# Optimization experiments

Hardware: AMD Instinct MI355X
Metric: run time of the kernel (lower is better)

Reference implementation:

```python
import jax, jax.numpy as jnp
import numpy as np
import math
from jax import lax

A_BICUBIC = -0.75  # PyTorch bicubic coefficient


def _bicubic_resize_matrix(out_n, in_n):
    """Dense [out_n, in_n] matrix implementing 1D bicubic resize (half-pixel,
    align_corners=False, border-replicated taps) exactly like F.interpolate."""
    a = A_BICUBIC
    src = (np.arange(out_n) + 0.5) * (in_n / out_n) - 0.5
    i0 = np.floor(src).astype(np.int64)
    t = src - i0
    M = np.zeros((out_n, in_n), dtype=np.float32)
    for k in range(-1, 3):
        idx = np.clip(i0 + k, 0, in_n - 1)
        d = np.abs(t - k)
        w = np.where(d <= 1.0, (a + 2) * d**3 - (a + 3) * d**2 + 1.0,
                     np.where(d < 2.0, a * d**3 - 5 * a * d**2 + 8 * a * d - 4 * a, 0.0))
        np.add.at(M, (np.arange(out_n), idx), w)
    return jnp.asarray(M)


def _relative_position_index(w):
    coords = np.stack(np.meshgrid(np.arange(w), np.arange(w), indexing='ij'))  # [2,w,w]
    cf = coords.reshape(2, -1)
    rel = (cf[:, :, None] - cf[:, None, :]).transpose(1, 2, 0)  # [w^2,w^2,2]
    rel[..., 0] += w - 1
    rel[..., 1] += w - 1
    rel[..., 0] *= 2 * w - 1
    return rel.sum(-1)  # [w^2, w^2]


def _grid_sample_bilinear(img, grid):
    """img: [G,d,Hi,Wi]; grid: [G,Ho,Wo,2] (x,y) in [-1,1].
    Bilinear, padding_mode='zeros', align_corners=False."""
    G, d, Hi, Wi = img.shape
    Ho, Wo = grid.shape[1:3]
    gx = (grid[..., 0] + 1.0) * (Wi * 0.5) - 0.5
    gy = (grid[..., 1] + 1.0) * (Hi * 0.5) - 0.5
    x0 = jnp.floor(gx)
    y0 = jnp.floor(gy)
    imgf = img.reshape(G, d, Hi * Wi)
    out = jnp.zeros((G, d, Ho * Wo), img.dtype)
    for dy in (0, 1):
        for dx in (0, 1):
            xi = x0 + dx
            yi = y0 + dy
            w = (1.0 - jnp.abs(gx - xi)) * (1.0 - jnp.abs(gy - yi))
            valid = (xi >= 0) & (xi < Wi) & (yi >= 0) & (yi < Hi)
            xic = jnp.clip(xi, 0, Wi - 1).astype(jnp.int32)
            yic = jnp.clip(yi, 0, Hi - 1).astype(jnp.int32)
            flat = (yic * Wi + xic).reshape(G, 1, Ho * Wo)
            v = jnp.take_along_axis(imgf, flat, axis=2)  # [G,d,HoWo]
            out = out + v * (w * valid).reshape(G, 1, Ho * Wo)
    return out.reshape(G, d, Ho, Wo)


def deformable_attention(x, q_w, q_b, k_w, k_b, v_w, v_b, o_w, o_b, dw_w, dw_b, off_w, bias_table, offset_scale=2.0):
    B, N, C = x.shape
    H = W = int(math.sqrt(N))
    heads = off_w.shape[0] // 2
    hd = C // heads
    wsz = (int(math.isqrt(bias_table.shape[0])) + 1) // 2  # (2w-1)^2 -> w

    xi = x.reshape(B, H, W, C).transpose(0, 3, 1, 2)  # [B,C,H,W]

    def conv1x1(t, w, b=None):
        y = jnp.einsum('bchw,oc->bohw', t, w)
        return y if b is None else y + b[None, :, None, None]

    Q = conv1x1(xi, q_w, q_b)
    K = conv1x1(xi, k_w, k_b)
    V = conv1x1(xi, v_w, v_b)

    # offset network: depthwise 5x5 conv -> GELU -> 1x1 -> tanh -> *scale
    h = lax.conv_general_dilated(xi, dw_w, (1, 1), 'SAME', feature_group_count=C,
                                 dimension_numbers=('NCHW', 'OIHW', 'NCHW'))
    h = jax.nn.gelu(h + dw_b[None, :, None, None], approximate=False)
    offsets = jnp.tanh(conv1x1(h, off_w)) * offset_scale  # [B,2*heads,H,W]
    offsets = offsets.reshape(B, heads, 2, H, W).transpose(0, 1, 3, 4, 2)  # [B,n,H,W,2]

    gy, gx = jnp.meshgrid(jnp.linspace(-1.0, 1.0, H), jnp.linspace(-1.0, 1.0, W), indexing='ij')
    grid = jnp.stack((gx, gy), axis=-1)  # [H,W,2]
    samp = jnp.clip(grid[None, None] + offsets, -1.0, 1.0).reshape(B * heads, H, W, 2)

    Kh = K.reshape(B * heads, hd, H, W)
    Vh = V.reshape(B * heads, hd, H, W)
    Ks = _grid_sample_bilinear(Kh, samp).reshape(B, heads, hd, N).transpose(0, 1, 3, 2)  # [B,n,N,d]
    Vs = _grid_sample_bilinear(Vh, samp).reshape(B, heads, hd, N).transpose(0, 1, 3, 2)
    Qh = Q.reshape(B, heads, hd, N).transpose(0, 1, 3, 2)  # [B,n,N,d]

    scores = jnp.einsum('bhid,bhjd->bhij', Qh, Ks) / math.sqrt(hd)

    # relative bias: table lookup on static index, bicubic upsample w^2 -> N
    rpi = _relative_position_index(wsz)  # static numpy [w^2,w^2]
    bias0 = bias_table[jnp.asarray(rpi.reshape(-1)), 0].reshape(wsz * wsz, wsz * wsz)
    M = _bicubic_resize_matrix(N, wsz * wsz)
    bias = M @ bias0 @ M.T  # [N,N]
    scores = scores + bias[None, None]

    probs = jax.nn.softmax(scores, axis=-1)
    out = jnp.einsum('bhij,bhjd->bhid', probs, Vs)  # [B,n,N,d]
    out = out.transpose(0, 1, 3, 2).reshape(B, C, H, W)  # b (h d) p q
    out = conv1x1(out, o_w, o_b)
    return out.reshape(B, C, N).transpose(0, 2, 1)  # [B,N,C]


def setup_inputs() -> dict:
    key = jax.random.key(0)
    ks = jax.random.split(key, 16)
    B, N, C = 4, 1024, 512
    heads, wsz, kk = 8, 8, 5
    s = 0.02
    return {
        'x': jax.random.normal(ks[0], (B, N, C), jnp.float32),
        'q_w': jax.random.normal(ks[1], (C, C), jnp.float32) * s,
        'q_b': jax.random.normal(ks[2], (C,), jnp.float32) * s,
        'k_w': jax.random.normal(ks[3], (C, C), jnp.float32) * s,
        'k_b': jax.random.normal(ks[4], (C,), jnp.float32) * s,
        'v_w': jax.random.normal(ks[5], (C, C), jnp.float32) * s,
        'v_b': jax.random.normal(ks[6], (C,), jnp.float32) * s,
        'o_w': jax.random.normal(ks[7], (C, C), jnp.float32) * s,
        'o_b': jax.random.normal(ks[8], (C,), jnp.float32) * s,
        'dw_w': jax.random.normal(ks[9], (C, 1, kk, kk), jnp.float32) * s,
        'dw_b': jax.random.normal(ks[10], (C,), jnp.float32) * s,
        'off_w': jax.random.normal(ks[11], (2 * heads, C), jnp.float32) * s,
        'bias_table': jax.random.normal(ks[12], ((2 * wsz - 1) ** 2, 1), jnp.float32),
    }


def reference(x, q_w, q_b, k_w, k_b, v_w, v_b, o_w, o_b, dw_w, dw_b, off_w, bias_table):
    return deformable_attention(x, q_w, q_b, k_w, k_b, v_w, v_b, o_w, o_b, dw_w, dw_b, off_w, bias_table)
```

## Files before the change

kernel.cpp:

```cpp
#include <hip/hip_runtime.h>
#include <math.h>

typedef unsigned short ushort;
typedef __attribute__((ext_vector_type(8))) short bf16x8;
typedef __attribute__((ext_vector_type(4))) float f32x4;

#define MFMA16(a, b, c) __builtin_amdgcn_mfma_f32_16x16x32_bf16(a, b, c, 0, 0, 0)
#define GLOAD16(g, l)                                                   \
  __builtin_amdgcn_global_load_lds(                                     \
      (const __attribute__((address_space(1))) unsigned int*)(g),       \
      (__attribute__((address_space(3))) unsigned int*)(l), 16, 0, 0)

__device__ __forceinline__ ushort f2bf(float f) {
  unsigned u = __float_as_uint(f);
  u += 0x7FFFu + ((u >> 16) & 1u);
  return (ushort)(u >> 16);
}
__device__ __forceinline__ float bf2f(ushort b) {
  return __uint_as_float(((unsigned)b) << 16);
}
__device__ __forceinline__ unsigned pk_bf16(float a, float b) {
  unsigned u;
  asm("v_cvt_pk_bf16_f32 %0, %1, %2" : "=v"(u) : "v"(a), "v"(b));
  return u;
}

__global__ __launch_bounds__(256) void split_hi(
    const float* __restrict__ in, ushort* __restrict__ hi, int n4) {
  int i = blockIdx.x * 256 + threadIdx.x;
  if (i >= n4) return;
  float4 v = ((const float4*)in)[i];
  ushort4 h;
  h.x = f2bf(v.x); h.y = f2bf(v.y); h.z = f2bf(v.z); h.w = f2bf(v.w);
  ((ushort4*)hi)[i] = h;
}

__global__ __launch_bounds__(256) void prep_weights(
    const float* __restrict__ q_w, const float* __restrict__ k_w,
    const float* __restrict__ v_w, const float* __restrict__ o_w,
    const float* __restrict__ dw_w, ushort* __restrict__ Wq,
    ushort* __restrict__ Wk, ushort* __restrict__ Wv,
    ushort* __restrict__ Woh, ushort* __restrict__ Wol,
    float* __restrict__ dwT) {
  int blk = blockIdx.x;
  if (blk < 1024) {
    int grp = blk >> 8;
    int i = (blk & 255) * 256 + threadIdx.x;
    if (grp < 3) {
      const float* in = grp == 0 ? q_w : grp == 1 ? k_w : v_w;
      ushort* hi = grp == 0 ? Wq : grp == 1 ? Wk : Wv;
      float4 v = ((const float4*)in)[i];
      ushort4 h;
      h.x = f2bf(v.x); h.y = f2bf(v.y); h.z = f2bf(v.z); h.w = f2bf(v.w);
      ((ushort4*)hi)[i] = h;
    } else {
      float4 v = ((const float4*)o_w)[i];
      ushort4 h, l;
      h.x = f2bf(v.x); l.x = f2bf(v.x - bf2f(h.x));
      h.y = f2bf(v.y); l.y = f2bf(v.y - bf2f(h.y));
      h.z = f2bf(v.z); l.z = f2bf(v.z - bf2f(h.z));
      h.w = f2bf(v.w); l.w = f2bf(v.w - bf2f(h.w));
      ((ushort4*)Woh)[i] = h;
      ((ushort4*)Wol)[i] = l;
    }
  } else {
    int c = (blk - 1024) * 256 + threadIdx.x;
    #pragma unroll
    for (int k = 0; k < 25; ++k) dwT[k * 512 + c] = dw_w[c * 25 + k];
  }
}

__global__ __launch_bounds__(256) void gemm_qkv(
    const ushort* __restrict__ X, const ushort* __restrict__ Wq,
    const ushort* __restrict__ Wk, const ushort* __restrict__ Wv,
    const float* __restrict__ b0, const float* __restrict__ b1,
    const float* __restrict__ b2, ushort* __restrict__ Qo,
    ushort* __restrict__ Ko, ushort* __restrict__ Vo) {
  __shared__ ushort lds[12288];
  ushort* sA = lds;
  ushort* sB = lds + 8192;
  int which = blockIdx.x >> 3;
  int n0 = (blockIdx.x & 7) * 64;
  int m0 = blockIdx.y * 128;
  const ushort* W; const float* bb; ushort* Y; float scale;
  if (which == 0)      { W = Wq; bb = b0; Y = Qo; scale = 0.125f; }
  else if (which == 1) { W = Wk; bb = b1; Y = Ko; scale = 1.0f; }
  else                 { W = Wv; bb = b2; Y = Vo; scale = 1.0f; }

  int tid = threadIdx.x;
  int lane = tid & 63;
  int w = tid >> 6;
  int wr = (w >> 1) * 64;
  int wc = (w & 1) * 32;
  int l8r = lane >> 3;
  int sll = ((lane & 7) ^ l8r) << 3;
  int l16 = lane & 15, lq = lane >> 4;

  f32x4 acc[4][2];
  f32x4 zero = {0.f, 0.f, 0.f, 0.f};
  #pragma unroll
  for (int m = 0; m < 4; ++m)
    #pragma unroll
    for (int n = 0; n < 2; ++n) acc[m][n] = zero;

  for (int kt = 0; kt < 8; ++kt) {
    int kk = kt * 64;
    __syncthreads();
    #pragma unroll
    for (int q = 0; q < 4; ++q) {
      int ci = w * 4 + q;
      GLOAD16(X + (size_t)(m0 + ci * 8 + l8r) * 512 + kk + sll, sA + ci * 512);
    }
    #pragma unroll
    for (int q = 0; q < 2; ++q) {
      int ci = w * 2 + q;
      GLOAD16(W + (size_t)(n0 + ci * 8 + l8r) * 512 + kk + sll, sB + ci * 512);
    }
    __syncthreads();
    #pragma unroll
    for (int ks = 0; ks < 2; ++ks) {
      int slot = ks * 4 + lq;
      bf16x8 a[4], bvv[2];
      #pragma unroll
      for (int m = 0; m < 4; ++m) {
        int r = wr + m * 16 + l16;
        a[m] = *(const bf16x8*)&sA[r * 64 + ((slot ^ (r & 7)) << 3)];
      }
      #pragma unroll
      for (int n = 0; n < 2; ++n) {
        int r = wc + n * 16 + l16;
        bvv[n] = *(const bf16x8*)&sB[r * 64 + ((slot ^ (r & 7)) << 3)];
      }
      #pragma unroll
      for (int m = 0; m < 4; ++m)
        #pragma unroll
        for (int n = 0; n < 2; ++n)
          acc[m][n] = MFMA16(a[m], bvv[n], acc[m][n]);
    }
  }
  #pragma unroll
  for (int n = 0; n < 2; ++n) {
    int col = n0 + wc + n * 16 + l16;
    float bv = bb[col];
    #pragma unroll
    for (int m = 0; m < 4; ++m) {
      #pragma unroll
      for (int j = 0; j < 4; ++j) {
        int row = m0 + wr + m * 16 + lq * 4 + j;
        Y[(size_t)row * 512 + col] = f2bf((acc[m][n][j] + bv) * scale);
      }
    }
  }
}

__global__ __launch_bounds__(256) void gemm_mfma(
    const ushort* __restrict__ Ahi, const ushort* __restrict__ Alo,
    const ushort* __restrict__ Bhi, const ushort* __restrict__ Blo,
    const float* __restrict__ bias, float* __restrict__ Y) {
  __shared__ ushort lds[24576];
  ushort* sAhi = lds;
  ushort* sAlo = lds + 8192;
  ushort* sBhi = lds + 16384;
  ushort* sBlo = lds + 20480;
  int m0 = blockIdx.y * 128, n0 = blockIdx.x * 64;
  int tid = threadIdx.x;
  int lane = tid & 63;
  int w = tid >> 6;
  int wr = (w >> 1) * 64;
  int wc = (w & 1) * 32;
  int l8r = lane >> 3;
  int sll = ((lane & 7) ^ l8r) << 3;
  int l16 = lane & 15, lq = lane >> 4;

  f32x4 acc[4][2];
  f32x4 zero = {0.f, 0.f, 0.f, 0.f};
  #pragma unroll
  for (int m = 0; m < 4; ++m)
    #pragma unroll
    for (int n = 0; n < 2; ++n) acc[m][n] = zero;

  for (int kt = 0; kt < 8; ++kt) {
    int kk = kt * 64;
    __syncthreads();
    #pragma unroll
    for (int q = 0; q < 4; ++q) {
      int ci = w * 4 + q;
      size_t go = (size_t)(m0 + ci * 8 + l8r) * 512 + kk + sll;
      GLOAD16(Ahi + go, sAhi + ci * 512);
      GLOAD16(Alo + go, sAlo + ci * 512);
    }
    #pragma unroll
    for (int q = 0; q < 2; ++q) {
      int ci = w * 2 + q;
      size_t go = (size_t)(n0 + ci * 8 + l8r) * 512 + kk + sll;
      GLOAD16(Bhi + go, sBhi + ci * 512);
      GLOAD16(Blo + go, sBlo + ci * 512);
    }
    __syncthreads();
    #pragma unroll
    for (int ks = 0; ks < 2; ++ks) {
      int slot = ks * 4 + lq;
      bf16x8 ah[4], al[4], bh[2], bl[2];
      #pragma unroll
      for (int m = 0; m < 4; ++m) {
        int r = wr + m * 16 + l16;
        int ph = (slot ^ (r & 7)) << 3;
        ah[m] = *(const bf16x8*)&sAhi[r * 64 + ph];
        al[m] = *(const bf16x8*)&sAlo[r * 64 + ph];
      }
      #pragma unroll
      for (int n = 0; n < 2; ++n) {
        int r = wc + n * 16 + l16;
        int ph = (slot ^ (r & 7)) << 3;
        bh[n] = *(const bf16x8*)&sBhi[r * 64 + ph];
        bl[n] = *(const bf16x8*)&sBlo[r * 64 + ph];
      }
      #pragma unroll
      for (int m = 0; m < 4; ++m)
        #pragma unroll
        for (int n = 0; n < 2; ++n) {
          acc[m][n] = MFMA16(ah[m], bh[n], acc[m][n]);
          acc[m][n] = MFMA16(ah[m], bl[n], acc[m][n]);
          acc[m][n] = MFMA16(al[m], bh[n], acc[m][n]);
        }
    }
  }
  #pragma unroll
  for (int n = 0; n < 2; ++n) {
    int col = n0 + wc + n * 16 + l16;
    float bv = bias[col];
    #pragma unroll
    for (int m = 0; m < 4; ++m) {
      #pragma unroll
      for (int j = 0; j < 4; ++j) {
        int row = m0 + wr + m * 16 + lq * 4 + j;
        Y[(size_t)row * 512 + col] = acc[m][n][j] + bv;
      }
    }
  }
}

__global__ __launch_bounds__(256) void offset_net2(
    const float* __restrict__ x, const float* __restrict__ dwT,
    const float* __restrict__ dw_b, const float* __restrict__ off_w,
    float* __restrict__ samp) {
  __shared__ float wT[16][516];
  __shared__ float hT[16][516];
  __shared__ float ofs[16][16];
  int x0 = blockIdx.x * 16;
  int y = blockIdx.y;
  int b = blockIdx.z;
  int tid = threadIdx.x;

  for (int e = tid; e < 2048; e += 256) {
    int o = e >> 7, c4 = e & 127;
    *(float4*)&wT[o][c4 * 4] = *(const float4*)&off_w[o * 512 + c4 * 4];
  }

  int c = tid * 2;
  float2 dwv[25];
  #pragma unroll
  for (int k = 0; k < 25; ++k) dwv[k] = *(const float2*)&dwT[k * 512 + c];
  float2 cb = *(const float2*)&dw_b[c];

  const float* xb = x + (size_t)b * 1024 * 512 + c;
  bool rv[5];
  #pragma unroll
  for (int r = 0; r < 5; ++r) {
    int yy = y - 2 + r;
    rv[r] = (yy >= 0 && yy < 32);
  }
  float2 win[5][5];
  #pragma unroll
  for (int j = 0; j < 4; ++j) {
    int xc = x0 - 2 + j;
    bool cvld = (xc >= 0 && xc < 32);
    #pragma unroll
    for (int r = 0; r < 5; ++r) {
      win[r][j] = (rv[r] && cvld)
          ? *(const float2*)&xb[(size_t)((y - 2 + r) * 32 + xc) * 512]
          : make_float2(0.f, 0.f);
    }
  }
  #pragma unroll
  for (int i = 0; i < 16; ++i) {
    int xc = x0 + i + 2;
    bool cvld = (xc < 32);
    #pragma unroll
    for (int r = 0; r < 5; ++r) {
      win[r][4] = (rv[r] && cvld)
          ? *(const float2*)&xb[(size_t)((y - 2 + r) * 32 + xc) * 512]
          : make_float2(0.f, 0.f);
    }
    float sx = cb.x, sy = cb.y;
    #pragma unroll
    for (int r = 0; r < 5; ++r)
      #pragma unroll
      for (int j = 0; j < 5; ++j) {
        sx += win[r][j].x * dwv[r * 5 + j].x;
        sy += win[r][j].y * dwv[r * 5 + j].y;
      }
    float g0 = 0.5f * sx * (1.0f + erff(sx * 0.70710678118654752f));
    float g1 = 0.5f * sy * (1.0f + erff(sy * 0.70710678118654752f));
    *(float2*)&hT[i][c] = make_float2(g0, g1);
    #pragma unroll
    for (int r = 0; r < 5; ++r) {
      win[r][0] = win[r][1]; win[r][1] = win[r][2];
      win[r][2] = win[r][3]; win[r][3] = win[r][4];
    }
  }
  __syncthreads();

  {
    int o = tid & 15, px = tid >> 4;
    float acc = 0.f;
    #pragma unroll 4
    for (int c4 = 0; c4 < 128; ++c4) {
      float4 hv = *(const float4*)&hT[px][c4 * 4];
      float4 wv = *(const float4*)&wT[o][c4 * 4];
      acc += hv.x * wv.x + hv.y * wv.y + hv.z * wv.z + hv.w * wv.w;
    }
    ofs[px][o] = tanhf(acc) * 2.0f;
  }
  __syncthreads();

  if (tid < 128) {
    int px = tid >> 3, h = tid & 7;
    int n = y * 32 + x0 + px;
    float gx = -1.0f + 2.0f * (float)(x0 + px) / 31.0f;
    float gy = -1.0f + 2.0f * (float)y / 31.0f;
    float sx = fminf(fmaxf(gx + ofs[px][2 * h], -1.0f), 1.0f);
    float sy = fminf(fmaxf(gy + ofs[px][2 * h + 1], -1.0f), 1.0f);
    float2 pc;
    pc.x = (sx + 1.0f) * 16.0f - 0.5f;
    pc.y = (sy + 1.0f) * 16.0f - 0.5f;
    ((float2*)samp)[(size_t)(b * 8 + h) * 1024 + n] = pc;
  }
}

__global__ __launch_bounds__(256) void grid_sample(
    const ushort* __restrict__ K, const ushort* __restrict__ V,
    const float* __restrict__ samp, ushort* __restrict__ Ks,
    ushort* __restrict__ Vt) {
  __shared__ ushort sV[64][72];
  int bh = blockIdx.y;
  int b = bh >> 3, h = bh & 7;
  int jb = blockIdx.x;
  int d = threadIdx.x & 63;
  for (int p = 0; p < 16; ++p) {
    int jl = p * 4 + (threadIdx.x >> 6);
    int j = jb * 64 + jl;
    float2 pc = ((const float2*)samp)[(size_t)bh * 1024 + j];
    float gx = pc.x, gy = pc.y;
    float x0 = floorf(gx), y0 = floorf(gy);
    float aK = 0.f, aV = 0.f;
    #pragma unroll
    for (int dy = 0; dy < 2; ++dy)
      #pragma unroll
      for (int dx = 0; dx < 2; ++dx) {
        float xi = x0 + (float)dx, yi = y0 + (float)dy;
        float wgt = (1.0f - fabsf(gx - xi)) * (1.0f - fabsf(gy - yi));
        if (xi >= 0.f && xi < 32.f && yi >= 0.f && yi < 32.f) {
          size_t base = ((size_t)b * 1024 + (int)yi * 32 + (int)xi) * 512 + h * 64 + d;
          aK += bf2f(K[base]) * wgt;
          aV += bf2f(V[base]) * wgt;
        }
      }
    Ks[((size_t)bh * 1024 + j) * 64 + d] = f2bf(aK);
    sV[jl][d] = f2bf(aV);
  }
  __syncthreads();
  int dd = threadIdx.x >> 2, c4 = threadIdx.x & 3;
  bf16x8 v0, v1;
  #pragma unroll
  for (int k = 0; k < 8; ++k) v0[k] = (short)sV[c4 * 16 + k][dd];
  #pragma unroll
  for (int k = 0; k < 8; ++k) v1[k] = (short)sV[c4 * 16 + 8 + k][dd];
  size_t o = ((size_t)bh * 64 + dd) * 1024 + jb * 64 + c4 * 16;
  *(bf16x8*)&Vt[o] = v0;
  *(bf16x8*)&Vt[o + 8] = v1;
}

__device__ __forceinline__ void bicubic_taps(int i, float* w, int* idx) {
  const float a = -0.75f;
  float src = ((float)i + 0.5f) * 0.0625f - 0.5f;
  float fi = floorf(src);
  int i0 = (int)fi;
  float t = src - fi;
  #pragma unroll
  for (int k = -1; k <= 2; ++k) {
    float d = fabsf(t - (float)k);
    float wv;
    if (d <= 1.0f)
      wv = ((a + 2.0f) * d - (a + 3.0f)) * d * d + 1.0f;
    else if (d < 2.0f)
      wv = a * (((d - 5.0f) * d + 8.0f) * d - 4.0f);
    else
      wv = 0.0f;
    int ic = i0 + k;
    ic = ic < 0 ? 0 : (ic > 63 ? 63 : ic);
    w[k + 1] = wv;
    idx[k + 1] = ic;
  }
}

__global__ __launch_bounds__(256) void bias_kernel(
    const float* __restrict__ table, float* __restrict__ bias) {
  __shared__ float tab[225];
  int i = blockIdx.x;
  int tid = threadIdx.x;
  if (tid < 225) tab[tid] = table[tid];
  __syncthreads();
  float wA[4]; int iA[4];
  bicubic_taps(i, wA, iA);
  for (int j = tid; j < 1024; j += 256) {
    float wB[4]; int iB[4];
    bicubic_taps(j, wB, iB);
    float sum = 0.f;
    #pragma unroll
    for (int ka = 0; ka < 4; ++ka) {
      int pa = iA[ka];
      int py = pa >> 3, px = pa & 7;
      float wa = wA[ka];
      #pragma unroll
      for (int kb = 0; kb < 4; ++kb) {
        int qb = iB[kb];
        int qy = qb >> 3, qx = qb & 7;
        sum += wa * wB[kb] * tab[(py - qy + 7) * 15 + (px - qx + 7)];
      }
    }
    bias[(size_t)i * 1024 + j] = sum;
  }
}

__global__ __launch_bounds__(512, 6) void attn_mfma(
    const ushort* __restrict__ Qh, const ushort* __restrict__ Ks,
    const ushort* __restrict__ Vt, const float* __restrict__ bias,
    ushort* __restrict__ Oh, ushort* __restrict__ Ol) {
  __shared__ ushort sK[2][2][2048];
  __shared__ ushort sVt[2][2][2048];
  __shared__ ushort sP[8][640];

  int tid = threadIdx.x;
  int lane = tid & 63;
  int w = tid >> 6;
  int qg = w & 3;
  int kvh = w >> 2;
  int l16 = lane & 15, lq = lane >> 4;
  int blk = blockIdx.x;
  int xcd = blk & 7;
  int rr = blk >> 3;
  int bh = ((rr & 3) << 3) + xcd;
  int i0 = (rr >> 2) * 64;
  int b = bh >> 3, h = bh & 7;

  bf16x8 qh[2];
  #pragma unroll
  for (int s = 0; s < 2; ++s)
    qh[s] = *(const bf16x8*)&Qh[((size_t)b * 1024 + i0 + qg * 16 + l16) * 512 +
                                h * 64 + s * 32 + lq * 8];

  f32x4 oacc[4];
  f32x4 zero = {0.f, 0.f, 0.f, 0.f};
  #pragma unroll
  for (int n = 0; n < 4; ++n) oacc[n] = zero;
  float mq = -INFINITY, lsum = 0.f;

  ushort* myP = sP[w];
  int krow = qg * 8 + (lane >> 3);
  int kslot = (lane & 7) ^ (krow & 7);
  int vrow = qg * 16 + (lane >> 2);
  int vslot = (lane & 3) ^ (vrow & 3);
  size_t kbase = ((size_t)bh * 1024 + kvh * 512 + krow) * 64 + kslot * 8;
  size_t vbase = ((size_t)bh * 64 + vrow) * 1024 + kvh * 512 + vslot * 8;
  ushort* dK0 = &sK[0][kvh][qg * 8 * 64];  ushort* dK1 = &sK[1][kvh][qg * 8 * 64];
  ushort* dV0 = &sVt[0][kvh][qg * 16 * 32]; ushort* dV1 = &sVt[1][kvh][qg * 16 * 32];
  const float* bprow = bias + (size_t)(i0 + qg * 16 + l16) * 1024 + kvh * 512;

  GLOAD16(Ks + kbase, dK0);
  GLOAD16(Vt + vbase, dV0);
  f32x4 bias_c[2];
  #pragma unroll
  for (int n = 0; n < 2; ++n)
    bias_c[n] = *(const f32x4*)&bprow[n * 16 + lq * 4];
  __syncthreads();

  int cur = 0;
  for (int t = 0; t < 16; ++t) {
    if (t < 15) {
      size_t off = (size_t)(t + 1) * 32;
      GLOAD16(Ks + kbase + off * 64, cur ? dK0 : dK1);
      GLOAD16(Vt + vbase + off, cur ? dV0 : dV1);
    }
    f32x4 sacc[2];
    #pragma unroll
    for (int n = 0; n < 2; ++n) sacc[n] = bias_c[n];
    if (t < 15) {
      #pragma unroll
      for (int n = 0; n < 2; ++n)
        bias_c[n] = *(const f32x4*)&bprow[(t + 1) * 32 + n * 16 + lq * 4];
    }
    const ushort* k_t = sK[cur][kvh];
    __builtin_amdgcn_s_setprio(1);
    #pragma unroll
    for (int ks = 0; ks < 2; ++ks) {
      int cslot = ((ks * 4 + lq) ^ (l16 & 7)) * 8;
      #pragma unroll
      for (int n = 0; n < 2; ++n) {
        bf16x8 aK = *(const bf16x8*)&k_t[(n * 16 + l16) * 64 + cslot];
        sacc[n] = MFMA16(aK, qh[ks], sacc[n]);
      }
    }
    __builtin_amdgcn_s_setprio(0);
    float mt = fmaxf(fmaxf(fmaxf(sacc[0][0], sacc[0][1]), fmaxf(sacc[0][2], sacc[0][3])),
                     fmaxf(fmaxf(sacc[1][0], sacc[1][1]), fmaxf(sacc[1][2], sacc[1][3])));
    mt = fmaxf(mt, __shfl_xor(mt, 16));
    mt = fmaxf(mt, __shfl_xor(mt, 32));
    if (!__all(mt <= mq + 8.0f)) {
      float mn = fmaxf(mq, mt);
      float sc = __expf(mq - mn);
      mq = mn;
      lsum *= sc;
      float scq[4];
      #pragma unroll
      for (int r = 0; r < 4; ++r) scq[r] = __shfl(sc, lq * 4 + r);
      #pragma unroll
      for (int n = 0; n < 4; ++n)
        #pragma unroll
        for (int r = 0; r < 4; ++r) oacc[n][r] *= scq[r];
    }
    float ts = 0.f;
    #pragma unroll
    for (int n = 0; n < 2; ++n) {
      float p0 = __expf(sacc[n][0] - mq);
      float p1 = __expf(sacc[n][1] - mq);
      float p2 = __expf(sacc[n][2] - mq);
      float p3 = __expf(sacc[n][3] - mq);
      ts += (p0 + p1) + (p2 + p3);
      uint2 u = make_uint2(pk_bf16(p0, p1), pk_bf16(p2, p3));
      *(uint2*)&myP[l16 * 40 + n * 16 + lq * 4] = u;
    }
    ts += __shfl_xor(ts, 16);
    ts += __shfl_xor(ts, 32);
    lsum += ts;
    bf16x8 pa = *(const bf16x8*)&myP[l16 * 40 + lq * 8];
    const ushort* vt_t = sVt[cur][kvh];
    __builtin_amdgcn_s_setprio(1);
    #pragma unroll
    for (int n = 0; n < 4; ++n) {
      int row = n * 16 + l16;
      bf16x8 bv = *(const bf16x8*)&vt_t[row * 32 + ((lq ^ (row & 3)) * 8)];
      oacc[n] = MFMA16(pa, bv, oacc[n]);
    }
    __builtin_amdgcn_s_setprio(0);
    __syncthreads();
    cur ^= 1;
  }

  float* mO = (float*)sK;
  float* mML = (float*)sVt;
  if (w >= 4) {
    int base = ((w - 4) * 64 + lane) * 16;
    #pragma unroll
    for (int n = 0; n < 4; ++n)
      #pragma unroll
      for (int r = 0; r < 4; ++r) mO[base + n * 4 + r] = oacc[n][r];
    mML[((w - 4) * 64 + lane) * 2 + 0] = mq;
    mML[((w - 4) * 64 + lane) * 2 + 1] = lsum;
  }
  __syncthreads();
  if (w < 4) {
    float mB = mML[(w * 64 + lane) * 2 + 0];
    float lB = mML[(w * 64 + lane) * 2 + 1];
    float mS = fmaxf(mq, mB);
    float fA = __expf(mq - mS), fB = __expf(mB - mS);
    float linv = 1.0f / (lsum * fA + lB * fB);
    float cAv = fA * linv, cBv = fB * linv;
    float cA[4], cB[4];
    #pragma unroll
    for (int r = 0; r < 4; ++r) {
      cA[r] = __shfl(cAv, lq * 4 + r);
      cB[r] = __shfl(cBv, lq * 4 + r);
    }
    int base = (w * 64 + lane) * 16;
    #pragma unroll
    for (int r = 0; r < 4; ++r) {
      int qr = i0 + qg * 16 + lq * 4 + r;
      #pragma unroll
      for (int n = 0; n < 4; ++n) {
        float v = oacc[n][r] * cA[r] + mO[base + n * 4 + r] * cB[r];
        ushort hb = f2bf(v);
        size_t o = ((size_t)b * 1024 + qr) * 512 + h * 64 + n * 16 + l16;
        Oh[o] = hb;
        Ol[o] = f2bf(v - bf2f(hb));
      }
    }
  }
}

extern "C" void kernel_launch(void* const* d_in, const int* in_sizes, int n_in,
                              void* d_out, int out_size, void* d_ws, size_t ws_size,
                              hipStream_t stream) {
  const float* x     = (const float*)d_in[0];
  const float* q_w   = (const float*)d_in[1];
  const float* q_b   = (const float*)d_in[2];
  const float* k_w   = (const float*)d_in[3];
  const float* k_b   = (const float*)d_in[4];
  const float* v_w   = (const float*)d_in[5];
  const float* v_b   = (const float*)d_in[6];
  const float* o_w   = (const float*)d_in[7];
  const float* o_b   = (const float*)d_in[8];
  const float* dw_w  = (const float*)d_in[9];
  const float* dw_b  = (const float*)d_in[10];
  const float* off_w = (const float*)d_in[11];
  const float* btab  = (const float*)d_in[12];

  float* ws = (float*)d_ws;
  const size_t SZ = (size_t)4 * 1024 * 512;
  float* bias = ws;
  float* samp = ws + 1048576;
  float* dwT  = ws + 1048576 + 65536;

  ushort* u = (ushort*)(dwT + 12800);
  ushort* Xh  = u;
  ushort* Qb  = Xh + SZ;
  ushort* Kb  = Qb + SZ;
  ushort* Vb  = Kb + SZ;
  ushort* Ksb = Vb + SZ;
  ushort* Vtr = Ksb + SZ;
  ushort* Aoh = Vtr + SZ;
  ushort* Aol = Aoh + SZ;
  ushort* Wq  = Aol + SZ;
  ushort* Wk  = Wq + 262144;
  ushort* Wv  = Wk + 262144;
  ushort* Woh = Wv + 262144;
  ushort* Wol = Woh + 262144;

  split_hi<<<2048, 256, 0, stream>>>(x, Xh, 524288);
  prep_weights<<<1026, 256, 0, stream>>>(q_w, k_w, v_w, o_w, dw_w, Wq, Wk, Wv,
                                         Woh, Wol, dwT);

  gemm_qkv<<<dim3(24, 32), 256, 0, stream>>>(Xh, Wq, Wk, Wv, q_b, k_b, v_b,
                                             Qb, Kb, Vb);

  offset_net2<<<dim3(2, 32, 4), 256, 0, stream>>>(x, dwT, dw_b, off_w, samp);
  bias_kernel<<<1024, 256, 0, stream>>>(btab, bias);
  grid_sample<<<dim3(16, 32), 256, 0, stream>>>(Kb, Vb, samp, Ksb, Vtr);

  attn_mfma<<<512, 512, 0, stream>>>(Qb, Ksb, Vtr, bias, Aoh, Aol);

  gemm_mfma<<<dim3(8, 32), 256, 0, stream>>>(Aoh, Aol, Woh, Wol, o_b,
                                             (float*)d_out);
}
```

Measured before the change: 120.9 us.

## Merge prep kernels, drop attention output low part, store bias as bf16

```diff
diff --git a/kernel.cpp b/kernel.cpp
--- a/kernel.cpp
+++ b/kernel.cpp
@@ -25,27 +25,24 @@
   return u;
 }
 
-__global__ __launch_bounds__(256) void split_hi(
-    const float* __restrict__ in, ushort* __restrict__ hi, int n4) {
-  int i = blockIdx.x * 256 + threadIdx.x;
-  if (i >= n4) return;
-  float4 v = ((const float4*)in)[i];
-  ushort4 h;
-  h.x = f2bf(v.x); h.y = f2bf(v.y); h.z = f2bf(v.z); h.w = f2bf(v.w);
-  ((ushort4*)hi)[i] = h;
-}
-
-__global__ __launch_bounds__(256) void prep_weights(
-    const float* __restrict__ q_w, const float* __restrict__ k_w,
-    const float* __restrict__ v_w, const float* __restrict__ o_w,
-    const float* __restrict__ dw_w, ushort* __restrict__ Wq,
-    ushort* __restrict__ Wk, ushort* __restrict__ Wv,
-    ushort* __restrict__ Woh, ushort* __restrict__ Wol,
-    float* __restrict__ dwT) {
+__global__ __launch_bounds__(256) void prep_all(
+    const float* __restrict__ x, const float* __restrict__ q_w,
+    const float* __restrict__ k_w, const float* __restrict__ v_w,
+    const float* __restrict__ o_w, const float* __restrict__ dw_w,
+    ushort* __restrict__ Xh, ushort* __restrict__ Wq, ushort* __restrict__ Wk,
+    ushort* __restrict__ Wv, ushort* __restrict__ Woh,
+    ushort* __restrict__ Wol, float* __restrict__ dwT) {
   int blk = blockIdx.x;
-  if (blk < 1024) {
-    int grp = blk >> 8;
-    int i = (blk & 255) * 256 + threadIdx.x;
+  if (blk < 2048) {
+    int i = blk * 256 + threadIdx.x;
+    float4 v = ((const float4*)x)[i];
+    ushort4 h;
+    h.x = f2bf(v.x); h.y = f2bf(v.y); h.z = f2bf(v.z); h.w = f2bf(v.w);
+    ((ushort4*)Xh)[i] = h;
+  } else if (blk < 3072) {
+    int blk2 = blk - 2048;
+    int grp = blk2 >> 8;
+    int i = (blk2 & 255) * 256 + threadIdx.x;
     if (grp < 3) {
       const float* in = grp == 0 ? q_w : grp == 1 ? k_w : v_w;
       ushort* hi = grp == 0 ? Wq : grp == 1 ? Wk : Wv;
@@ -64,7 +61,7 @@
       ((ushort4*)Wol)[i] = l;
     }
   } else {
-    int c = (blk - 1024) * 256 + threadIdx.x;
+    int c = (blk - 3072) * 256 + threadIdx.x;
     #pragma unroll
     for (int k = 0; k < 25; ++k) dwT[k * 512 + c] = dw_w[c * 25 + k];
   }
@@ -153,29 +150,27 @@
   }
 }
 
-__global__ __launch_bounds__(256) void gemm_mfma(
-    const ushort* __restrict__ Ahi, const ushort* __restrict__ Alo,
-    const ushort* __restrict__ Bhi, const ushort* __restrict__ Blo,
-    const float* __restrict__ bias, float* __restrict__ Y) {
-  __shared__ ushort lds[24576];
-  ushort* sAhi = lds;
-  ushort* sAlo = lds + 8192;
-  ushort* sBhi = lds + 16384;
-  ushort* sBlo = lds + 20480;
-  int m0 = blockIdx.y * 128, n0 = blockIdx.x * 64;
+__global__ __launch_bounds__(256) void gemm_o(
+    const ushort* __restrict__ A, const ushort* __restrict__ Wh,
+    const ushort* __restrict__ Wl, const float* __restrict__ bias,
+    float* __restrict__ Y) {
+  __shared__ ushort sA[4096];
+  __shared__ ushort sWh[4096];
+  __shared__ ushort sWl[4096];
+  int m0 = blockIdx.y * 64, n0 = blockIdx.x * 64;
   int tid = threadIdx.x;
   int lane = tid & 63;
   int w = tid >> 6;
-  int wr = (w >> 1) * 64;
+  int wr = (w >> 1) * 32;
   int wc = (w & 1) * 32;
   int l8r = lane >> 3;
   int sll = ((lane & 7) ^ l8r) << 3;
   int l16 = lane & 15, lq = lane >> 4;
 
-  f32x4 acc[4][2];
+  f32x4 acc[2][2];
   f32x4 zero = {0.f, 0.f, 0.f, 0.f};
   #pragma unroll
-  for (int m = 0; m < 4; ++m)
+  for (int m = 0; m < 2; ++m)
     #pragma unroll
     for (int n = 0; n < 2; ++n) acc[m][n] = zero;
 
@@ -183,45 +178,37 @@
     int kk = kt * 64;
     __syncthreads();
     #pragma unroll
-    for (int q = 0; q < 4; ++q) {
-      int ci = w * 4 + q;
-      size_t go = (size_t)(m0 + ci * 8 + l8r) * 512 + kk + sll;
-      GLOAD16(Ahi + go, sAhi + ci * 512);
-      GLOAD16(Alo + go, sAlo + ci * 512);
-    }
-    #pragma unroll
     for (int q = 0; q < 2; ++q) {
       int ci = w * 2 + q;
-      size_t go = (size_t)(n0 + ci * 8 + l8r) * 512 + kk + sll;
-      GLOAD16(Bhi + go, sBhi + ci * 512);
-      GLOAD16(Blo + go, sBlo + ci * 512);
+      size_t ga = (size_t)(m0 + ci * 8 + l8r) * 512 + kk + sll;
+      GLOAD16(A + ga, sA + ci * 512);
+      size_t gw = (size_t)(n0 + ci * 8 + l8r) * 512 + kk + sll;
+      GLOAD16(Wh + gw, sWh + ci * 512);
+      GLOAD16(Wl + gw, sWl + ci * 512);
     }
     __syncthreads();
     #pragma unroll
     for (int ks = 0; ks < 2; ++ks) {
       int slot = ks * 4 + lq;
-      bf16x8 ah[4], al[4], bh[2], bl[2];
-      #pragma unroll
-      for (int m = 0; m < 4; ++m) {
+      bf16x8 a[2], bh[2], bl[2];
+      #pragma unroll
+      for (int m = 0; m < 2; ++m) {
         int r = wr + m * 16 + l16;
-        int ph = (slot ^ (r & 7)) << 3;
-        ah[m] = *(const bf16x8*)&sAhi[r * 64 + ph];
-        al[m] = *(const bf16x8*)&sAlo[r * 64 + ph];
+        a[m] = *(const bf16x8*)&sA[r * 64 + ((slot ^ (r & 7)) << 3)];
       }
       #pragma unroll
       for (int n = 0; n < 2; ++n) {
         int r = wc + n * 16 + l16;
         int ph = (slot ^ (r & 7)) << 3;
-        bh[n] = *(const bf16x8*)&sBhi[r * 64 + ph];
-        bl[n] = *(const bf16x8*)&sBlo[r * 64 + ph];
-      }
-      #pragma unroll
-      for (int m = 0; m < 4; ++m)
+        bh[n] = *(const bf16x8*)&sWh[r * 64 + ph];
+        bl[n] = *(const bf16x8*)&sWl[r * 64 + ph];
+      }
+      #pragma unroll
+      for (int m = 0; m < 2; ++m)
         #pragma unroll
         for (int n = 0; n < 2; ++n) {
-          acc[m][n] = MFMA16(ah[m], bh[n], acc[m][n]);
-          acc[m][n] = MFMA16(ah[m], bl[n], acc[m][n]);
-          acc[m][n] = MFMA16(al[m], bh[n], acc[m][n]);
+          acc[m][n] = MFMA16(a[m], bh[n], acc[m][n]);
+          acc[m][n] = MFMA16(a[m], bl[n], acc[m][n]);
         }
     }
   }
@@ -230,7 +217,7 @@
     int col = n0 + wc + n * 16 + l16;
     float bv = bias[col];
     #pragma unroll
-    for (int m = 0; m < 4; ++m) {
+    for (int m = 0; m < 2; ++m) {
       #pragma unroll
       for (int j = 0; j < 4; ++j) {
         int row = m0 + wr + m * 16 + lq * 4 + j;
@@ -405,7 +392,7 @@
 }
 
 __global__ __launch_bounds__(256) void bias_kernel(
-    const float* __restrict__ table, float* __restrict__ bias) {
+    const float* __restrict__ table, ushort* __restrict__ bias) {
   __shared__ float tab[225];
   int i = blockIdx.x;
   int tid = threadIdx.x;
@@ -429,14 +416,14 @@
         sum += wa * wB[kb] * tab[(py - qy + 7) * 15 + (px - qx + 7)];
       }
     }
-    bias[(size_t)i * 1024 + j] = sum;
+    bias[(size_t)i * 1024 + j] = f2bf(sum);
   }
 }
 
 __global__ __launch_bounds__(512, 6) void attn_mfma(
     const ushort* __restrict__ Qh, const ushort* __restrict__ Ks,
-    const ushort* __restrict__ Vt, const float* __restrict__ bias,
-    ushort* __restrict__ Oh, ushort* __restrict__ Ol) {
+    const ushort* __restrict__ Vt, const ushort* __restrict__ bias,
+    ushort* __restrict__ Oh) {
   __shared__ ushort sK[2][2][2048];
   __shared__ ushort sVt[2][2][2048];
   __shared__ ushort sP[8][640];
@@ -475,14 +462,14 @@
   size_t vbase = ((size_t)bh * 64 + vrow) * 1024 + kvh * 512 + vslot * 8;
   ushort* dK0 = &sK[0][kvh][qg * 8 * 64];  ushort* dK1 = &sK[1][kvh][qg * 8 * 64];
   ushort* dV0 = &sVt[0][kvh][qg * 16 * 32]; ushort* dV1 = &sVt[1][kvh][qg * 16 * 32];
-  const float* bprow = bias + (size_t)(i0 + qg * 16 + l16) * 1024 + kvh * 512;
+  const ushort* bprow = bias + (size_t)(i0 + qg * 16 + l16) * 1024 + kvh * 512;
 
   GLOAD16(Ks + kbase, dK0);
   GLOAD16(Vt + vbase, dV0);
-  f32x4 bias_c[2];
+  ushort4 bias_c[2];
   #pragma unroll
   for (int n = 0; n < 2; ++n)
-    bias_c[n] = *(const f32x4*)&bprow[n * 16 + lq * 4];
+    bias_c[n] = *(const ushort4*)&bprow[n * 16 + lq * 4];
   __syncthreads();
 
   int cur = 0;
@@ -494,11 +481,16 @@
     }
     f32x4 sacc[2];
     #pragma unroll
-    for (int n = 0; n < 2; ++n) sacc[n] = bias_c[n];
+    for (int n = 0; n < 2; ++n) {
+      sacc[n][0] = bf2f(bias_c[n].x);
+      sacc[n][1] = bf2f(bias_c[n].y);
+      sacc[n][2] = bf2f(bias_c[n].z);
+      sacc[n][3] = bf2f(bias_c[n].w);
+    }
     if (t < 15) {
       #pragma unroll
       for (int n = 0; n < 2; ++n)
-        bias_c[n] = *(const f32x4*)&bprow[(t + 1) * 32 + n * 16 + lq * 4];
+        bias_c[n] = *(const ushort4*)&bprow[(t + 1) * 32 + n * 16 + lq * 4];
     }
     const ushort* k_t = sK[cur][kvh];
     __builtin_amdgcn_s_setprio(1);
@@ -589,10 +581,8 @@
       #pragma unroll
       for (int n = 0; n < 4; ++n) {
         float v = oacc[n][r] * cA[r] + mO[base + n * 4 + r] * cB[r];
-        ushort hb = f2bf(v);
         size_t o = ((size_t)b * 1024 + qr) * 512 + h * 64 + n * 16 + l16;
-        Oh[o] = hb;
-        Ol[o] = f2bf(v - bf2f(hb));
+        Oh[o] = f2bf(v);
       }
     }
   }
@@ -617,38 +607,35 @@
 
   float* ws = (float*)d_ws;
   const size_t SZ = (size_t)4 * 1024 * 512;
-  float* bias = ws;
-  float* samp = ws + 1048576;
-  float* dwT  = ws + 1048576 + 65536;
+  float* samp = ws;
+  float* dwT  = ws + 65536;
 
   ushort* u = (ushort*)(dwT + 12800);
-  ushort* Xh  = u;
-  ushort* Qb  = Xh + SZ;
-  ushort* Kb  = Qb + SZ;
-  ushort* Vb  = Kb + SZ;
-  ushort* Ksb = Vb + SZ;
-  ushort* Vtr = Ksb + SZ;
-  ushort* Aoh = Vtr + SZ;
-  ushort* Aol = Aoh + SZ;
-  ushort* Wq  = Aol + SZ;
-  ushort* Wk  = Wq + 262144;
-  ushort* Wv  = Wk + 262144;
-  ushort* Woh = Wv + 262144;
-  ushort* Wol = Woh + 262144;
-
-  split_hi<<<2048, 256, 0, stream>>>(x, Xh, 524288);
-  prep_weights<<<1026, 256, 0, stream>>>(q_w, k_w, v_w, o_w, dw_w, Wq, Wk, Wv,
-                                         Woh, Wol, dwT);
+  ushort* Xh   = u;
+  ushort* Qb   = Xh + SZ;
+  ushort* Kb   = Qb + SZ;
+  ushort* Vb   = Kb + SZ;
+  ushort* Ksb  = Vb + SZ;
+  ushort* Vtr  = Ksb + SZ;
+  ushort* Aoh  = Vtr + SZ;
+  ushort* biasb = Aoh + SZ;
+  ushort* Wq   = biasb + 1048576;
+  ushort* Wk   = Wq + 262144;
+  ushort* Wv   = Wk + 262144;
+  ushort* Woh  = Wv + 262144;
+  ushort* Wol  = Woh + 262144;
+
+  prep_all<<<3074, 256, 0, stream>>>(x, q_w, k_w, v_w, o_w, dw_w, Xh, Wq, Wk,
+                                     Wv, Woh, Wol, dwT);
 
   gemm_qkv<<<dim3(24, 32), 256, 0, stream>>>(Xh, Wq, Wk, Wv, q_b, k_b, v_b,
                                              Qb, Kb, Vb);
 
   offset_net2<<<dim3(2, 32, 4), 256, 0, stream>>>(x, dwT, dw_b, off_w, samp);
-  bias_kernel<<<1024, 256, 0, stream>>>(btab, bias);
+  bias_kernel<<<1024, 256, 0, stream>>>(btab, biasb);
   grid_sample<<<dim3(16, 32), 256, 0, stream>>>(Kb, Vb, samp, Ksb, Vtr);
 
-  attn_mfma<<<512, 512, 0, stream>>>(Qb, Ksb, Vtr, bias, Aoh, Aol);
-
-  gemm_mfma<<<dim3(8, 32), 256, 0, stream>>>(Aoh, Aol, Woh, Wol, o_b,
-                                             (float*)d_out);
-}
+  attn_mfma<<<512, 512, 0, stream>>>(Qb, Ksb, Vtr, biasb, Aoh);
+
+  gemm_o<<<dim3(8, 64), 256, 0, stream>>>(Aoh, Woh, Wol, o_b, (float*)d_out);
+}
```

Measured after the change: 109.9 us. -9.2%, faster.
